# Kernel tuning notes

Hardware: AMD Instinct MI355X
Metric: run time of the kernel (lower is better)

The kernel has to match this reference:

```python
import jax, jax.numpy as jnp
import numpy as np

N_NODES = 100000
N_EDGES = 1600000
N_GRAPHS = 64
D_IN, D_HID, D_OUT = 128, 256, 128


def gcn_conv(x, src, dst, W, b, n_nodes):
    """PyG-style GCNConv: x @ W, add self-loops, sym-normalize, scatter-add src->dst, + bias."""
    h = x @ W  # (N, out)
    loop = jnp.arange(n_nodes, dtype=src.dtype)
    src_f = jnp.concatenate([src, loop])
    dst_f = jnp.concatenate([dst, loop])
    deg = jax.ops.segment_sum(jnp.ones_like(dst_f, dtype=h.dtype), dst_f, num_segments=n_nodes)
    dinv = jnp.where(deg > 0, jax.lax.rsqrt(deg), 0.0)
    norm = dinv[src_f] * dinv[dst_f]  # (E+N,)
    msg = h[src_f] * norm[:, None]    # (E+N, out)  -- dominant memory traffic
    out = jax.ops.segment_sum(msg, dst_f, num_segments=n_nodes)
    return out + b


def setup_inputs() -> dict:
    key = jax.random.key(0)
    k1, k2, k3, k4, k5 = jax.random.split(key, 5)
    x = jax.random.normal(k1, (N_NODES, D_IN), dtype=jnp.float32)
    edge_index = jax.random.randint(k2, (2, N_EDGES), 0, N_NODES, dtype=jnp.int64)
    batch = jnp.sort(jax.random.randint(k3, (N_NODES,), 0, N_GRAPHS, dtype=jnp.int64))
    W1 = jax.random.normal(k4, (D_IN, D_HID), dtype=jnp.float32) * (1.0 / np.sqrt(D_IN))
    b1 = jnp.zeros((D_HID,), dtype=jnp.float32)
    W2 = jax.random.normal(k5, (D_HID, D_OUT), dtype=jnp.float32) * (1.0 / np.sqrt(D_HID))
    b2 = jnpps = jnp.zeros((D_OUT,), dtype=jnp.float32)
    return {"x": x, "edge_index": edge_index, "batch": batch,
            "W1": W1, "b1": b1, "W2": W2, "b2": b2}


def reference(x, edge_index, batch, W1, b1, W2, b2):
    src, dst = edge_index[0], edge_index[1]
    n = x.shape[0]
    h = gcn_conv(x, src, dst, W1, b1, n)
    h = jax.nn.relu(h)
    h = gcn_conv(h, src, dst, W2, b2, n)
    # global_add_pool
    return jax.ops.segment_sum(h, batch, num_segments=N_GRAPHS)
```

## Files before the change

kernel.cpp:

```cpp
#include <hip/hip_runtime.h>

#define NN 100000
#define NNPAD 100352
#define NE 1600000
#define NG 64
#define DI 128
#define DH 256
#define DO 128
#define SEG2 25088
#define NPART 256
#define PSTRIDE 392
#define PCAP 7168
#define PB 391

using short8 = __attribute__((ext_vector_type(8))) short;
using f32x4  = __attribute__((ext_vector_type(4))) float;

__device__ __forceinline__ float bf2f(unsigned short u) {
    return __uint_as_float(((unsigned)u) << 16);
}
__device__ __forceinline__ unsigned short f2bf(float f) {
    unsigned u = __float_as_uint(f);
    unsigned r = (u + 0x7FFFu + ((u >> 16) & 1u)) >> 16;
    return (unsigned short)r;
}

__global__ __launch_bounds__(256) void k_prep(const float* __restrict__ x,
        unsigned short* __restrict__ xbf, const float* __restrict__ W1,
        unsigned short* __restrict__ w1t, const int* __restrict__ src,
        const int* __restrict__ dst, int* __restrict__ pcur, int2* __restrict__ pe) {
    int t = threadIdx.x;
    if (blockIdx.x < PB) {
        __shared__ int hist[NPART];
        __shared__ int curb[NPART];
        const int EPT = 16;
        hist[t] = 0;
        __syncthreads();
        int base = blockIdx.x * (256 * EPT) + t;
        int sA[EPT], dA[EPT];
#pragma unroll
        for (int k = 0; k < EPT; ++k) {
            int i = base + k * 256;
            if (i < NE) {
                sA[k] = src[i]; dA[k] = dst[i];
                atomicAdd(&hist[dA[k] / PSTRIDE], 1);
            } else dA[k] = -1;
        }
        __syncthreads();
        curb[t] = t * PCAP + atomicAdd(&pcur[t], hist[t]);
        __syncthreads();
#pragma unroll
        for (int k = 0; k < EPT; ++k) {
            if (dA[k] >= 0) {
                int b = dA[k] / PSTRIDE;
                int pos = atomicAdd(&curb[b], 1);
                pe[pos] = make_int2(sA[k], dA[k]);
            }
        }
        return;
    }
    int i = (blockIdx.x - PB) * 256 + t;
    const int NX4 = NN * 32;
    if (i < NX4) {
        float4 v = ((const float4*)x)[i];
        ushort4 o;
        o.x = f2bf(v.x); o.y = f2bf(v.y); o.z = f2bf(v.z); o.w = f2bf(v.w);
        ((ushort4*)xbf)[i] = o;
    } else if (i < NX4 + DI * DH) {
        int tt = i - NX4;
        int k = tt / DH, n = tt % DH;
        w1t[n * DI + k] = f2bf(W1[tt]);
    }
}

__global__ __launch_bounds__(256) void k_count(const int2* __restrict__ pe,
        const int* __restrict__ pcur, int* __restrict__ cnt,
        int* __restrict__ rowst, int* __restrict__ pt) {
    __shared__ int c[512];
    int p = blockIdx.x;
    int lo = p * PSTRIDE;
    int t = threadIdx.x;
    c[t] = 0; c[t + 256] = 0;
    __syncthreads();
    int j1 = p * PCAP + pcur[p];
    for (int j = p * PCAP + t; j < j1; j += 256)
        atomicAdd(&c[pe[j].y - lo], 1);
    __syncthreads();
    int cc0 = c[t], cc1 = c[t + 256];
    for (int off = 1; off < 512; off <<= 1) {
        int v0 = (t >= off) ? c[t - off] : 0;
        int v1 = (t + 256 >= off) ? c[t + 256 - off] : 0;
        __syncthreads();
        c[t] += v0; c[t + 256] += v1;
        __syncthreads();
    }
    if (t < PSTRIDE) {
        int d = lo + t;
        if (d < NN) { cnt[d] = cc0; rowst[d] = c[t] - cc0; }
    }
    if (t + 256 < PSTRIDE) {
        int d = lo + t + 256;
        if (d < NN) { cnt[d] = cc1; rowst[d] = c[t + 256] - cc1; }
    }
    if (t == 0) pt[p] = c[511];
}

__global__ void k_scan2p(int* __restrict__ pt, int* __restrict__ cntg) {
    __shared__ int sh[256];
    int t = threadIdx.x;
    if (t < NG) cntg[t] = 0;
    int v = pt[t];
    sh[t] = v;
    __syncthreads();
    for (int off = 1; off < 256; off <<= 1) {
        int add = (t >= off) ? sh[t - off] : 0;
        __syncthreads();
        sh[t] += add;
        __syncthreads();
    }
    pt[t] = sh[t] - v;
}

__global__ void k_scan3(int* __restrict__ rowst, const int* __restrict__ pt,
                        const int* __restrict__ deg, float* __restrict__ dinv,
                        const int* __restrict__ batch, int2* __restrict__ gdv,
                        int* __restrict__ cntg, int n, int total) {
    __shared__ int sh[NG];
    int t = threadIdx.x;
    if (t < NG) sh[t] = 0;
    __syncthreads();
    int i = blockIdx.x * 256 + t;
    if (i < n) {
        float dv = rsqrtf((float)(deg[i] + 1));
        dinv[i] = dv;
        int b = batch[i];
        int2 g; g.x = __float_as_int(dv); g.y = b;
        gdv[i] = g;
        atomicAdd(&sh[b], 1);
        rowst[i] += pt[i / PSTRIDE];
    }
    if (i == 0) rowst[n] = total;
    __syncthreads();
    if (t < NG && sh[t]) atomicAdd(&cntg[t], sh[t]);
}

__global__ __launch_bounds__(256) void k_place(const int2* __restrict__ pe,
        const int* __restrict__ pcur, const int* __restrict__ rowst,
        const float* __restrict__ dinv, int2* __restrict__ csr8) {
    __shared__ int cur[PSTRIDE];
    __shared__ float dl[PSTRIDE];
    int p = blockIdx.x;
    int lo = p * PSTRIDE;
    int t = threadIdx.x;
    for (int i = t; i < PSTRIDE; i += 256) {
        int d = lo + i;
        cur[i] = (d < NN) ? rowst[d] : 0;
        dl[i]  = (d < NN) ? dinv[d] : 0.f;
    }
    __syncthreads();
    int j1 = p * PCAP + pcur[p];
    for (int j = p * PCAP + t; j < j1; j += 256) {
        int2 ed = pe[j];
        int a = ed.y - lo;
        float w = dinv[ed.x] * dl[a];
        int pos = atomicAdd(&cur[a], 1);
        csr8[pos] = make_int2(ed.x, __float_as_int(w));
    }
}

__global__ __launch_bounds__(256) void k_cmbuild(const int2* __restrict__ csr8,
        const int* __restrict__ rowst, const int* __restrict__ batch,
        const int2* __restrict__ gdv, float* __restrict__ cmT) {
    __shared__ float acc[SEG2];
    int g   = blockIdx.x >> 2;
    int seg = blockIdx.x & 3;
    int slo = seg * SEG2;
    int t = threadIdx.x;
    for (int i = t; i < SEG2; i += 256) acc[i] = 0.f;

    int lo = 0, hi = NN;
    while (lo < hi) { int m = (lo + hi) >> 1; if (batch[m] < g) lo = m + 1; else hi = m; }
    int dstart = lo;
    int lo2 = lo, hi2 = NN;
    while (lo2 < hi2) { int m = (lo2 + hi2) >> 1; if (batch[m] < g + 1) lo2 = m + 1; else hi2 = m; }
    int e0 = rowst[dstart], e1 = rowst[lo2];
    __syncthreads();

    int j = e0 + t;
    for (; j + 768 < e1; j += 1024) {
        int2 p0 = csr8[j];
        int2 p1 = csr8[j + 256];
        int2 p2 = csr8[j + 512];
        int2 p3 = csr8[j + 768];
        int a0 = p0.x - slo, a1 = p1.x - slo, a2 = p2.x - slo, a3 = p3.x - slo;
        if ((unsigned)a0 < SEG2) atomicAdd(&acc[a0], __int_as_float(p0.y));
        if ((unsigned)a1 < SEG2) atomicAdd(&acc[a1], __int_as_float(p1.y));
        if ((unsigned)a2 < SEG2) atomicAdd(&acc[a2], __int_as_float(p2.y));
        if ((unsigned)a3 < SEG2) atomicAdd(&acc[a3], __int_as_float(p3.y));
    }
    for (; j < e1; j += 256) {
        int2 p = csr8[j];
        int a = p.x - slo;
        if ((unsigned)a < SEG2) atomicAdd(&acc[a], __int_as_float(p.y));
    }
    __syncthreads();

    float* row = cmT + (size_t)g * NNPAD;
    for (int i = t; i < SEG2; i += 256) {
        int s = slo + i;
        float v = acc[i];
        if (s < NN) {
            int2 gv = gdv[s];
            if (gv.y == g) { float dv = __int_as_float(gv.x); v += dv * dv; }
        }
        row[s] = v;
    }
}

__global__ __launch_bounds__(256) void k_agg16(const unsigned short* __restrict__ feat,
        const int2* __restrict__ csr8, const int* __restrict__ row_start,
        const float* __restrict__ dinv, unsigned short* __restrict__ out, int n) {
    int gid = blockIdx.x * blockDim.x + threadIdx.x;
    int node = gid >> 4;
    int lane = threadIdx.x & 15;
    if (node >= n) return;
    const short8* f8 = (const short8*)feat;
    float wd = dinv[node];
    float wd2 = wd * wd;
    short8 a = f8[(size_t)node * 16 + lane];
    float acc[8];
#pragma unroll
    for (int i = 0; i < 8; ++i) acc[i] = bf2f((unsigned short)a[i]) * wd2;
    int j = row_start[node], end = row_start[node + 1];
    for (; j + 7 < end; j += 8) {
        int2 p0 = csr8[j],     p1 = csr8[j + 1], p2 = csr8[j + 2], p3 = csr8[j + 3];
        int2 p4 = csr8[j + 4], p5 = csr8[j + 5], p6 = csr8[j + 6], p7 = csr8[j + 7];
        short8 v0 = f8[(size_t)p0.x * 16 + lane];
        short8 v1 = f8[(size_t)p1.x * 16 + lane];
        short8 v2 = f8[(size_t)p2.x * 16 + lane];
        short8 v3 = f8[(size_t)p3.x * 16 + lane];
        short8 v4 = f8[(size_t)p4.x * 16 + lane];
        short8 v5 = f8[(size_t)p5.x * 16 + lane];
        short8 v6 = f8[(size_t)p6.x * 16 + lane];
        short8 v7 = f8[(size_t)p7.x * 16 + lane];
        float w0 = __int_as_float(p0.y), w1 = __int_as_float(p1.y);
        float w2 = __int_as_float(p2.y), w3 = __int_as_float(p3.y);
        float w4 = __int_as_float(p4.y), w5 = __int_as_float(p5.y);
        float w6 = __int_as_float(p6.y), w7 = __int_as_float(p7.y);
#pragma unroll
        for (int i = 0; i < 8; ++i)
            acc[i] += w0 * bf2f((unsigned short)v0[i]) + w1 * bf2f((unsigned short)v1[i])
                    + w2 * bf2f((unsigned short)v2[i]) + w3 * bf2f((unsigned short)v3[i])
                    + w4 * bf2f((unsigned short)v4[i]) + w5 * bf2f((unsigned short)v5[i])
                    + w6 * bf2f((unsigned short)v6[i]) + w7 * bf2f((unsigned short)v7[i]);
    }
    for (; j + 3 < end; j += 4) {
        int2 p0 = csr8[j], p1 = csr8[j + 1], p2 = csr8[j + 2], p3 = csr8[j + 3];
        float w0 = __int_as_float(p0.y), w1 = __int_as_float(p1.y);
        float w2 = __int_as_float(p2.y), w3 = __int_as_float(p3.y);
        short8 v0 = f8[(size_t)p0.x * 16 + lane];
        short8 v1 = f8[(size_t)p1.x * 16 + lane];
        short8 v2 = f8[(size_t)p2.x * 16 + lane];
        short8 v3 = f8[(size_t)p3.x * 16 + lane];
#pragma unroll
        for (int i = 0; i < 8; ++i)
            acc[i] += w0 * bf2f((unsigned short)v0[i]) + w1 * bf2f((unsigned short)v1[i])
                    + w2 * bf2f((unsigned short)v2[i]) + w3 * bf2f((unsigned short)v3[i]);
    }
    for (; j < end; ++j) {
        int2 p = csr8[j];
        float w = __int_as_float(p.y);
        short8 v = f8[(size_t)p.x * 16 + lane];
#pragma unroll
        for (int i = 0; i < 8; ++i) acc[i] += w * bf2f((unsigned short)v[i]);
    }
    short8 o;
#pragma unroll
    for (int i = 0; i < 8; ++i) o[i] = (short)f2bf(acc[i]);
    ((short8*)out)[(size_t)node * 16 + lane] = o;
}

__global__ __launch_bounds__(512) void k_fused(const unsigned short* __restrict__ agg1,
        const unsigned short* __restrict__ w1t, const float* __restrict__ b1,
        const float* __restrict__ cmT, float* __restrict__ partial) {
    __shared__ unsigned short Ws[256 * 128];
    __shared__ unsigned short As[64 * 128];
    __shared__ unsigned short Hs[256 * 64];
    __shared__ unsigned short Cs[64 * 64];

    const int tid = threadIdx.x;
    const int sb = blockIdx.x * 512;

#pragma unroll
    for (int i = 0; i < 8; ++i) {
        int c = tid + i * 512;
        int row = c >> 4, seg = c & 15;
        uint4 v = *(const uint4*)(w1t + row * 128 + seg * 8);
        *(uint4*)((char*)Ws + row * 256 + ((seg * 16) ^ ((row & 7) << 4))) = v;
    }

    const int w  = tid >> 6;
    const int l  = tid & 63;
    const int lr = l & 15;
    const int lg = l >> 4;
    const int swz = (lr & 7) << 4;
    const int j0 = w * 32;

    float bb0 = b1[j0 + lr];
    float bb1 = b1[j0 + 16 + lr];

    f32x4 acc2[4][2] = {};

    for (int c = 0; c < 8; ++c) {
        int s0 = sb + c * 64;
        __syncthreads();
#pragma unroll
        for (int i = 0; i < 2; ++i) {
            int cc = tid + i * 512;
            int row = cc >> 4, seg = cc & 15;
            uint4 v = make_uint4(0, 0, 0, 0);
            int node = s0 + row;
            if (node < NN) v = *(const uint4*)(agg1 + (size_t)node * 128 + seg * 8);
            *(uint4*)((char*)As + row * 256 + ((seg * 16) ^ ((row & 7) << 4))) = v;
        }
        {
            int g = tid >> 3, seg = tid & 7;
            const float* cp = cmT + (size_t)g * NNPAD + s0 + seg * 8;
            float4 f0 = *(const float4*)cp;
            float4 f1 = *(const float4*)(cp + 4);
            uint4 v;
            v.x = (unsigned)f2bf(f0.x) | ((unsigned)f2bf(f0.y) << 16);
            v.y = (unsigned)f2bf(f0.z) | ((unsigned)f2bf(f0.w) << 16);
            v.z = (unsigned)f2bf(f1.x) | ((unsigned)f2bf(f1.y) << 16);
            v.w = (unsigned)f2bf(f1.z) | ((unsigned)f2bf(f1.w) << 16);
            *(uint4*)((char*)Cs + g * 128 + ((seg * 16) ^ ((g & 7) << 4))) = v;
        }
        __syncthreads();

        f32x4 accA[4][2] = {};
#pragma unroll
        for (int ks = 0; ks < 4; ++ks) {
            int kb = ks * 64 + lg * 16;
            short8 a[4];
#pragma unroll
            for (int m = 0; m < 4; ++m)
                a[m] = *(const short8*)((const char*)As + (m * 16 + lr) * 256 + (kb ^ swz));
#pragma unroll
            for (int n = 0; n < 2; ++n) {
                short8 b = *(const short8*)((const char*)Ws + (j0 + n * 16 + lr) * 256 + (kb ^ swz));
#pragma unroll
                for (int m = 0; m < 4; ++m)
                    accA[m][n] = __builtin_amdgcn_mfma_f32_16x16x32_bf16(a[m], b, accA[m][n], 0, 0, 0);
            }
        }
#pragma unroll
        for (int n = 0; n < 2; ++n) {
            int j = j0 + n * 16 + lr;
            float bbv = n ? bb1 : bb0;
#pragma unroll
            for (int m = 0; m < 4; ++m) {
                float v0 = fmaxf(accA[m][n][0] + bbv, 0.f);
                float v1 = fmaxf(accA[m][n][1] + bbv, 0.f);
                float v2 = fmaxf(accA[m][n][2] + bbv, 0.f);
                float v3 = fmaxf(accA[m][n][3] + bbv, 0.f);
                uint2 p;
                p.x = (unsigned)f2bf(v0) | ((unsigned)f2bf(v1) << 16);
                p.y = (unsigned)f2bf(v2) | ((unsigned)f2bf(v3) << 16);
                *(uint2*)((char*)Hs + j * 128 + (((m * 16 + lg * 4) * 2) ^ swz)) = p;
            }
        }
        __syncthreads();

#pragma unroll
        for (int ks = 0; ks < 2; ++ks) {
            int kb = ks * 64 + lg * 16;
            short8 a[4];
#pragma unroll
            for (int mg = 0; mg < 4; ++mg)
                a[mg] = *(const short8*)((const char*)Cs + (mg * 16 + lr) * 128 + (kb ^ swz));
#pragma unroll
            for (int n = 0; n < 2; ++n) {
                short8 b = *(const short8*)((const char*)Hs + (j0 + n * 16 + lr) * 128 + (kb ^ swz));
#pragma unroll
                for (int mg = 0; mg < 4; ++mg)
                    acc2[mg][n] = __builtin_amdgcn_mfma_f32_16x16x32_bf16(a[mg], b, acc2[mg][n], 0, 0, 0);
            }
        }
    }

    float* pb = partial + (size_t)blockIdx.x * (NG * DH);
#pragma unroll
    for (int mg = 0; mg < 4; ++mg)
#pragma unroll
        for (int n = 0; n < 2; ++n)
#pragma unroll
            for (int r = 0; r < 4; ++r) {
                int g = mg * 16 + lg * 4 + r;
                int j = j0 + n * 16 + lr;
                pb[g * DH + j] = acc2[mg][n][r];
            }
}

__global__ __launch_bounds__(256) void k_tail(const float* __restrict__ partial,
        const float* __restrict__ W2, const float* __restrict__ b2,
        const int* __restrict__ cntg, float* __restrict__ out) {
    __shared__ float pre[DH];
    int g = blockIdx.x;
    int t = threadIdx.x;
    float s0 = 0.f, s1 = 0.f, s2 = 0.f, s3 = 0.f;
    for (int b = 0; b < 196; b += 4) {
        s0 += partial[(size_t)b * (NG * DH) + g * DH + t];
        s1 += partial[(size_t)(b + 1) * (NG * DH) + g * DH + t];
        s2 += partial[(size_t)(b + 2) * (NG * DH) + g * DH + t];
        s3 += partial[(size_t)(b + 3) * (NG * DH) + g * DH + t];
    }
    pre[t] = (s0 + s1) + (s2 + s3);
    __syncthreads();
    if (t < DO) {
        float acc = (float)cntg[g] * b2[t];
        for (int k = 0; k < DH; ++k)
            acc = fmaf(pre[k], W2[k * DO + t], acc);
        out[g * DO + t] = acc;
    }
}


extern "C" void kernel_launch(void* const* d_in, const int* in_sizes, int n_in,
                              void* d_out, int out_size, void* d_ws, size_t ws_size,
                              hipStream_t stream) {
    const float* x     = (const float*)d_in[0];
    const int*   ei    = (const int*)d_in[1];
    const int*   batch = (const int*)d_in[2];
    const float* W1    = (const float*)d_in[3];
    const float* b1    = (const float*)d_in[4];
    const float* W2    = (const float*)d_in[5];
    const float* b2    = (const float*)d_in[6];
    float* out = (float*)d_out;

    const int* src = ei;
    const int* dst = ei + NE;

    char* ws = (char*)d_ws;
    float*          dinv    = (float*)(ws + 0);
    int*            cnt_in  = (int*)(ws + 524288);
    int*            rowst   = (int*)(ws + 1048576);
    int*            pt      = (int*)(ws + 1572864);
    int*            cntg    = (int*)(ws + 1576960);
    unsigned short* w1t     = (unsigned short*)(ws + 1577216);
    int2*           gdv     = (int2*)(ws + 1642752);
    int2*           csr8    = (int2*)(ws + 2443264);
    unsigned short* xbf     = (unsigned short*)(ws + 15243264);
    unsigned short* agg1    = (unsigned short*)(ws + 40843264);
    float*          cmT     = (float*)(ws + 66443264);
    float*          partial = (float*)(ws + 92133376);
    int2*           pe      = (int2*)(ws + 104978432);
    int*            pcur    = (int*)(ws + 119658496);

    const int BLK = 256;
    auto cdiv = [](int a, int b) { return (a + b - 1) / b; };
    const int NB = cdiv(NN, 256);

    hipMemsetAsync(pcur, 0, NPART * 4, stream);

    {
        int prep_blocks = cdiv(NN * 32 + DI * DH, BLK);
        k_prep<<<PB + prep_blocks, BLK, 0, stream>>>(x, xbf, W1, w1t, src, dst, pcur, pe);
    }

    k_count<<<NPART, 256, 0, stream>>>(pe, pcur, cnt_in, rowst, pt);

    k_scan2p<<<1, 256, 0, stream>>>(pt, cntg);
    k_scan3<<<NB, 256, 0, stream>>>(rowst, pt, cnt_in, dinv, batch, gdv, cntg, NN, NE);

    k_place<<<NPART, 256, 0, stream>>>(pe, pcur, rowst, dinv, csr8);

    k_cmbuild<<<NG * 4, 256, 0, stream>>>(csr8, rowst, batch, gdv, cmT);

    k_agg16<<<cdiv(NN * 16, BLK), BLK, 0, stream>>>(xbf, csr8, rowst, dinv, agg1, NN);

    k_fused<<<NNPAD / 512, 512, 0, stream>>>(agg1, w1t, b1, cmT, partial);

    k_tail<<<NG, 256, 0, stream>>>(partial, W2, b2, cntg, out);
}
```

Before: 229.3 us.

## Fold partition scan and degree normalization into count and place kernels

Removes the separate single-block scan kernel and the per-node scan3 kernel. Degree inverse, per-graph counts and the local row starts are now computed in k_count, and each k_place block redoes the 256-entry partition prefix scan to add its base offset. The 8-way unrolled gather loop in the aggregation kernel is also dropped, leaving only the 4-way loop. The aim is to cut two kernel launches and one pass over per-node arrays, at the cost of a redundant scan in every k_place block and possibly less memory-level parallelism in the gather.

```diff
diff --git a/kernel.cpp b/kernel.cpp
--- a/kernel.cpp
+++ b/kernel.cpp
@@ -74,13 +74,16 @@
 }
 
 __global__ __launch_bounds__(256) void k_count(const int2* __restrict__ pe,
-        const int* __restrict__ pcur, int* __restrict__ cnt,
+        const int* __restrict__ pcur, const int* __restrict__ batch,
+        float* __restrict__ dinv, int2* __restrict__ gdv, int* __restrict__ cntg,
         int* __restrict__ rowst, int* __restrict__ pt) {
     __shared__ int c[512];
+    __shared__ int sg[NG];
     int p = blockIdx.x;
     int lo = p * PSTRIDE;
     int t = threadIdx.x;
     c[t] = 0; c[t + 256] = 0;
+    if (t < NG) sg[t] = 0;
     __syncthreads();
     int j1 = p * PCAP + pcur[p];
     for (int j = p * PCAP + t; j < j1; j += 256)
@@ -94,68 +97,58 @@
         c[t] += v0; c[t + 256] += v1;
         __syncthreads();
     }
-    if (t < PSTRIDE) {
-        int d = lo + t;
-        if (d < NN) { cnt[d] = cc0; rowst[d] = c[t] - cc0; }
-    }
-    if (t + 256 < PSTRIDE) {
-        int d = lo + t + 256;
-        if (d < NN) { cnt[d] = cc1; rowst[d] = c[t + 256] - cc1; }
+#pragma unroll
+    for (int k = 0; k < 2; ++k) {
+        int i = t + k * 256;
+        if (i < PSTRIDE) {
+            int d = lo + i;
+            if (d < NN) {
+                int deg = k ? cc1 : cc0;
+                float dv = rsqrtf((float)(deg + 1));
+                dinv[d] = dv;
+                int b = batch[d];
+                gdv[d] = make_int2(__float_as_int(dv), b);
+                atomicAdd(&sg[b], 1);
+                rowst[d] = c[i] - deg;
+            }
+        }
     }
     if (t == 0) pt[p] = c[511];
-}
-
-__global__ void k_scan2p(int* __restrict__ pt, int* __restrict__ cntg) {
-    __shared__ int sh[256];
-    int t = threadIdx.x;
-    if (t < NG) cntg[t] = 0;
-    int v = pt[t];
-    sh[t] = v;
-    __syncthreads();
-    for (int off = 1; off < 256; off <<= 1) {
-        int add = (t >= off) ? sh[t - off] : 0;
-        __syncthreads();
-        sh[t] += add;
-        __syncthreads();
-    }
-    pt[t] = sh[t] - v;
-}
-
-__global__ void k_scan3(int* __restrict__ rowst, const int* __restrict__ pt,
-                        const int* __restrict__ deg, float* __restrict__ dinv,
-                        const int* __restrict__ batch, int2* __restrict__ gdv,
-                        int* __restrict__ cntg, int n, int total) {
-    __shared__ int sh[NG];
-    int t = threadIdx.x;
-    if (t < NG) sh[t] = 0;
-    __syncthreads();
-    int i = blockIdx.x * 256 + t;
-    if (i < n) {
-        float dv = rsqrtf((float)(deg[i] + 1));
-        dinv[i] = dv;
-        int b = batch[i];
-        int2 g; g.x = __float_as_int(dv); g.y = b;
-        gdv[i] = g;
-        atomicAdd(&sh[b], 1);
-        rowst[i] += pt[i / PSTRIDE];
-    }
-    if (i == 0) rowst[n] = total;
-    __syncthreads();
-    if (t < NG && sh[t]) atomicAdd(&cntg[t], sh[t]);
+    __syncthreads();
+    if (t < NG && sg[t]) atomicAdd(&cntg[t], sg[t]);
 }
 
 __global__ __launch_bounds__(256) void k_place(const int2* __restrict__ pe,
-        const int* __restrict__ pcur, const int* __restrict__ rowst,
-        const float* __restrict__ dinv, int2* __restrict__ csr8) {
+        const int* __restrict__ pcur, const int* __restrict__ pt,
+        int* __restrict__ rowst, const float* __restrict__ dinv,
+        int2* __restrict__ csr8) {
     __shared__ int cur[PSTRIDE];
     __shared__ float dl[PSTRIDE];
+    __shared__ int psc[NPART];
     int p = blockIdx.x;
     int lo = p * PSTRIDE;
     int t = threadIdx.x;
+    int v = pt[t];
+    psc[t] = v;
+    __syncthreads();
+    for (int off = 1; off < NPART; off <<= 1) {
+        int add = (t >= off) ? psc[t - off] : 0;
+        __syncthreads();
+        psc[t] += add;
+        __syncthreads();
+    }
+    int base = psc[p] - pt[p];
     for (int i = t; i < PSTRIDE; i += 256) {
         int d = lo + i;
-        cur[i] = (d < NN) ? rowst[d] : 0;
-        dl[i]  = (d < NN) ? dinv[d] : 0.f;
+        if (d < NN) {
+            int r = rowst[d] + base;
+            rowst[d] = r;
+            cur[i] = r;
+            dl[i]  = dinv[d];
+        } else {
+            cur[i] = 0; dl[i] = 0.f;
+            if (d == NN) rowst[NN] = NE;
+        }
     }
     __syncthreads();
     int j1 = p * PCAP + pcur[p];
@@ -232,28 +225,6 @@
 #pragma unroll
     for (int i = 0; i < 8; ++i) acc[i] = bf2f((unsigned short)a[i]) * wd2;
     int j = row_start[node], end = row_start[node + 1];
-    for (; j + 7 < end; j += 8) {
-        int2 p0 = csr8[j],     p1 = csr8[j + 1], p2 = csr8[j + 2], p3 = csr8[j + 3];
-        int2 p4 = csr8[j + 4], p5 = csr8[j + 5], p6 = csr8[j + 6], p7 = csr8[j + 7];
-        short8 v0 = f8[(size_t)p0.x * 16 + lane];
-        short8 v1 = f8[(size_t)p1.x * 16 + lane];
-        short8 v2 = f8[(size_t)p2.x * 16 + lane];
-        short8 v3 = f8[(size_t)p3.x * 16 + lane];
-        short8 v4 = f8[(size_t)p4.x * 16 + lane];
-        short8 v5 = f8[(size_t)p5.x * 16 + lane];
-        short8 v6 = f8[(size_t)p6.x * 16 + lane];
-        short8 v7 = f8[(size_t)p7.x * 16 + lane];
-        float w0 = __int_as_float(p0.y), w1 = __int_as_float(p1.y);
-        float w2 = __int_as_float(p2.y), w3 = __int_as_float(p3.y);
-        float w4 = __int_as_float(p4.y), w5 = __int_as_float(p5.y);
-        float w6 = __int_as_float(p6.y), w7 = __int_as_float(p7.y);
-#pragma unroll
-        for (int i = 0; i < 8; ++i)
-            acc[i] += w0 * bf2f((unsigned short)v0[i]) + w1 * bf2f((unsigned short)v1[i])
-                    + w2 * bf2f((unsigned short)v2[i]) + w3 * bf2f((unsigned short)v3[i])
-                    + w4 * bf2f((unsigned short)v4[i]) + w5 * bf2f((unsigned short)v5[i])
-                    + w6 * bf2f((unsigned short)v6[i]) + w7 * bf2f((unsigned short)v7[i]);
-    }
     for (; j + 3 < end; j += 4) {
         int2 p0 = csr8[j], p1 = csr8[j + 1], p2 = csr8[j + 2], p3 = csr8[j + 3];
         float w0 = __int_as_float(p0.y), w1 = __int_as_float(p1.y);
@@ -442,10 +413,8 @@
 
     char* ws = (char*)d_ws;
     float*          dinv    = (float*)(ws + 0);
-    int*            cnt_in  = (int*)(ws + 524288);
     int*            rowst   = (int*)(ws + 1048576);
     int*            pt      = (int*)(ws + 1572864);
-    int*            cntg    = (int*)(ws + 1576960);
     unsigned short* w1t     = (unsigned short*)(ws + 1577216);
     int2*           gdv     = (int2*)(ws + 1642752);
     int2*           csr8    = (int2*)(ws + 2443264);
@@ -455,24 +424,21 @@
     float*          partial = (float*)(ws + 92133376);
     int2*           pe      = (int2*)(ws + 104978432);
     int*            pcur    = (int*)(ws + 119658496);
+    int*            cntg    = (int*)(ws + 119659520);
 
     const int BLK = 256;
     auto cdiv = [](int a, int b) { return (a + b - 1) / b; };
-    const int NB = cdiv(NN, 256);
-
-    hipMemsetAsync(pcur, 0, NPART * 4, stream);
+
+    hipMemsetAsync(pcur, 0, NPART * 4 + NG * 4, stream);
 
     {
         int prep_blocks = cdiv(NN * 32 + DI * DH, BLK);
         k_prep<<<PB + prep_blocks, BLK, 0, stream>>>(x, xbf, W1, w1t, src, dst, pcur, pe);
     }
 
-    k_count<<<NPART, 256, 0, stream>>>(pe, pcur, cnt_in, rowst, pt);
-
-    k_scan2p<<<1, 256, 0, stream>>>(pt, cntg);
-    k_scan3<<<NB, 256, 0, stream>>>(rowst, pt, cnt_in, dinv, batch, gdv, cntg, NN, NE);
-
-    k_place<<<NPART, 256, 0, stream>>>(pe, pcur, rowst, dinv, csr8);
+    k_count<<<NPART, 256, 0, stream>>>(pe, pcur, batch, dinv, gdv, cntg, rowst, pt);
+
+    k_place<<<NPART, 256, 0, stream>>>(pe, pcur, pt, rowst, dinv, csr8);
 
     k_cmbuild<<<NG * 4, 256, 0, stream>>>(csr8, rowst, batch, gdv, cmT);
 
```

Measured after the change: 223.2 us. 1.03x faster.
